# Kernel optimization log

Hardware: AMD Instinct MI355X
Metric: run time of the kernel (lower is better)

The kernel has to match this reference:

```python
import jax, jax.numpy as jnp
import numpy as np

EPS = 1e-15  # matches torch_geometric dense pooling EPS


def gcn_conv(x, src, dst, w, W, b, n):
    # GCNConv(normalize=False): linear first, then weighted scatter-add src->dst, then bias
    h = x @ W
    msg = w[:, None] * h[src]  # [E, out]
    return jax.ops.segment_sum(msg, dst, num_segments=n) + b


def setup_inputs() -> dict:
    key = jax.random.key(0)
    ks = jax.random.split(key, 8)
    N, E, d, k = 12288, 393216, 256, 16
    x = jax.random.normal(ks[0], (N, d), dtype=jnp.float32)
    edge_index = jax.random.randint(ks[1], (2, E), 0, N, dtype=jnp.int32)
    edge_weight = jax.random.uniform(ks[2], (E,), dtype=jnp.float32)
    sc = 1.0 / np.sqrt(d).astype(np.float32)
    W1 = jax.random.normal(ks[3], (d, d), dtype=jnp.float32) * sc
    b1 = jnp.zeros((d,), jnp.float32)
    W2 = jax.random.normal(ks[4], (d, d), dtype=jnp.float32) * sc
    b2 = jnp.zeros((d,), jnp.float32)
    Wm = jax.random.normal(ks[5], (d, k), dtype=jnp.float32) * sc
    bm = jnp.zeros((k,), jnp.float32)
    return dict(x=x, edge_weight=edge_weight, W1=W1, b1=b1, W2=W2, b2=b2,
                Wm=Wm, bm=bm, edge_index=edge_index)


def reference(x, edge_weight, W1, b1, W2, b2, Wm, bm, edge_index):
    src, dst = edge_index[0], edge_index[1]
    n = x.shape[0]
    # message-passing stack: GCNConv -> ReLU -> GCNConv -> ReLU
    h = jax.nn.relu(gcn_conv(x, src, dst, edge_weight, W1, b1, n))
    h = jax.nn.relu(gcn_conv(h, src, dst, edge_weight, W2, b2, n))
    # cluster MLP (single Linear, Identity activations)
    s_logits = h @ Wm + bm  # [N, k]
    # to_dense_adj(edge_index, edge_attr=edge_weight): dense [N, N]
    adj = jnp.zeros((n, n), x.dtype).at[src, dst].add(edge_weight)
    # just_balance_pool (batch of 1)
    s = jax.nn.softmax(s_logits, axis=-1)  # [N, k]
    out = s.T @ h              # pooled features (unused by module output)
    out_adj = s.T @ adj @ s    # pooled adjacency (unused by module output)
    gram = s.T @ s             # [k, k]
    k = s.shape[-1]
    b_loss = -jnp.trace(jnp.sqrt(gram + EPS)) / jnp.sqrt(jnp.float32(n * k))
    return s, b_loss
```

## Files before the change

### kernel.cpp

```cpp
#include <hip/hip_runtime.h>
#include <hip/hip_bf16.h>
#include <hip/hip_fp16.h>

#define D 256
#define KCL 16
#define EPS 1e-15f
#define PAD 128

typedef __attribute__((ext_vector_type(8))) short short8;
typedef __attribute__((ext_vector_type(4))) float f32x4;

__device__ __forceinline__ short bfhi(float v) {
    __hip_bfloat16 b = __float2bfloat16(v);
    return __builtin_bit_cast(short, b);
}
__device__ __forceinline__ float bf2f(short s) {
    __hip_bfloat16 b = __builtin_bit_cast(__hip_bfloat16, s);
    return __bfloat162float(b);
}

__global__ __launch_bounds__(256) void setup_k(const float* __restrict__ W1,
                                               const float* __restrict__ W2,
                                               short* __restrict__ Wt1h, short* __restrict__ Wt1l,
                                               short* __restrict__ Wt2h, short* __restrict__ Wt2l,
                                               const int* __restrict__ src,
                                               const int* __restrict__ dst,
                                               const float* __restrict__ ew,
                                               int* __restrict__ deg,
                                               int2* __restrict__ edges, int E) {
    int b = blockIdx.x;
    if (b < 512) {
        const float* W = (b < 256) ? W1 : W2;
        short* Th = (b < 256) ? Wt1h : Wt2h;
        short* Tl = (b < 256) ? Wt1l : Wt2l;
        int c = b & 255;
        int k = threadIdx.x;
        float v = W[(size_t)k * D + c];
        short h = bfhi(v);
        Th[(size_t)c * D + k] = h;
        Tl[(size_t)c * D + k] = bfhi(v - bf2f(h));
    } else {
        int e = (b - 512) * 256 + threadIdx.x;
        if (e < E) {
            int d = dst[e];
            int slot = atomicAdd(&deg[d], 1);
            if (slot < PAD)
                edges[(size_t)d * PAD + slot] = make_int2(src[e], __float_as_int(ew[e]));
        }
    }
}

#define GBM 64
#define APAD 40
__global__ __launch_bounds__(256) void gemm_k(const float* __restrict__ A,
                                              const short* __restrict__ Bth,
                                              const short* __restrict__ Btl,
                                              __half* __restrict__ C) {
    __shared__ short Ah[GBM][APAD];
    __shared__ short Al[GBM][APAD];
    int tid = threadIdx.x;
    int lane = tid & 63, w = tid >> 6;
    int bm = blockIdx.x * GBM, bn = blockIdx.y * 64;
    f32x4 acc[4];
#pragma unroll
    for (int i = 0; i < 4; ++i) acc[i] = (f32x4){0.f, 0.f, 0.f, 0.f};

    int r  = tid >> 2;
    int cc = (tid & 3) * 8;
    int ar = w * 16 + (lane & 15);
    int kq = (lane >> 4) * 8;

    for (int kk = 0; kk < D; kk += 32) {
        const float* ap = &A[(size_t)(bm + r) * D + kk + cc];
        float4 v0 = *(const float4*)ap;
        float4 v1 = *(const float4*)(ap + 4);
        float vv[8] = {v0.x, v0.y, v0.z, v0.w, v1.x, v1.y, v1.z, v1.w};
        short8 hi, lo;
#pragma unroll
        for (int j = 0; j < 8; ++j) {
            short h = bfhi(vv[j]);
            hi[j] = h;
            lo[j] = bfhi(vv[j] - bf2f(h));
        }
        __syncthreads();
        *(short8*)&Ah[r][cc] = hi;
        *(short8*)&Al[r][cc] = lo;
        __syncthreads();

        short8 a_h = *(const short8*)&Ah[ar][kq];
        short8 a_l = *(const short8*)&Al[ar][kq];
#pragma unroll
        for (int nf = 0; nf < 4; ++nf) {
            int col = bn + nf * 16 + (lane & 15);
            short8 b_h = *(const short8*)&Bth[(size_t)col * D + kk + kq];
            short8 b_l = *(const short8*)&Btl[(size_t)col * D + kk + kq];
            acc[nf] = __builtin_amdgcn_mfma_f32_16x16x32_bf16(a_h, b_h, acc[nf], 0, 0, 0);
            acc[nf] = __builtin_amdgcn_mfma_f32_16x16x32_bf16(a_h, b_l, acc[nf], 0, 0, 0);
            acc[nf] = __builtin_amdgcn_mfma_f32_16x16x32_bf16(a_l, b_h, acc[nf], 0, 0, 0);
        }
    }
    int rbase = bm + w * 16 + (lane >> 4) * 4;
    int cb = bn + (lane & 15);
#pragma unroll
    for (int nf = 0; nf < 4; ++nf)
#pragma unroll
        for (int rr = 0; rr < 4; ++rr)
            C[(size_t)(rbase + rr) * D + cb + nf * 16] = __float2half(acc[nf][rr]);
}

__global__ __launch_bounds__(128) void spmm_k(const __half* __restrict__ h,
                                              const int2* __restrict__ edges,
                                              const int* __restrict__ deg,
                                              const float* __restrict__ bias,
                                              float* __restrict__ out) {
    int node = blockIdx.x;
    int t = threadIdx.x;
    int n = min(deg[node], PAD);
    __shared__ int2 se[PAD];
    if (t < n) se[t] = edges[(size_t)node * PAD + t];
    __syncthreads();
    const __half2* h2 = (const __half2*)h;
    float acc0 = 0.f, acc1 = 0.f;
    int i = 0;
    for (; i + 4 <= n; i += 4) {
        int2 e0 = se[i], e1 = se[i + 1], e2 = se[i + 2], e3 = se[i + 3];
        float2 a0 = __half22float2(h2[(size_t)e0.x * (D / 2) + t]);
        float2 a1 = __half22float2(h2[(size_t)e1.x * (D / 2) + t]);
        float2 a2 = __half22float2(h2[(size_t)e2.x * (D / 2) + t]);
        float2 a3 = __half22float2(h2[(size_t)e3.x * (D / 2) + t]);
        float w0 = __int_as_float(e0.y), w1 = __int_as_float(e1.y);
        float w2 = __int_as_float(e2.y), w3 = __int_as_float(e3.y);
        acc0 = fmaf(w0, a0.x, acc0); acc1 = fmaf(w0, a0.y, acc1);
        acc0 = fmaf(w1, a1.x, acc0); acc1 = fmaf(w1, a1.y, acc1);
        acc0 = fmaf(w2, a2.x, acc0); acc1 = fmaf(w2, a2.y, acc1);
        acc0 = fmaf(w3, a3.x, acc0); acc1 = fmaf(w3, a3.y, acc1);
    }
    for (; i < n; ++i) {
        int2 e = se[i];
        float2 a = __half22float2(h2[(size_t)e.x * (D / 2) + t]);
        float wv = __int_as_float(e.y);
        acc0 = fmaf(wv, a.x, acc0); acc1 = fmaf(wv, a.y, acc1);
    }
    float2 bv = *(const float2*)&bias[2 * t];
    *(float2*)&out[(size_t)node * D + 2 * t] =
        make_float2(fmaxf(acc0 + bv.x, 0.f), fmaxf(acc1 + bv.y, 0.f));
}

__global__ __launch_bounds__(256) void cluster_k(const float* __restrict__ h,
                                                 const float* __restrict__ Wm,
                                                 const float* __restrict__ bmv,
                                                 float* __restrict__ s_out,
                                                 float* __restrict__ partial) {
    __shared__ float dssq[4][KCL];
    int tid = threadIdx.x;
    int wave = tid >> 6, lane = tid & 63;
    int node = blockIdx.x * 4 + wave;

    float4 hv = *(const float4*)&h[(size_t)node * D + lane * 4];
    float p[KCL];
#pragma unroll
    for (int j = 0; j < KCL; ++j) p[j] = 0.f;
    const float* hp = (const float*)&hv;
#pragma unroll
    for (int u = 0; u < 4; ++u) {
        float hval = hp[u];
        const float4* wrow = (const float4*)&Wm[(size_t)(lane * 4 + u) * KCL];
#pragma unroll
        for (int q = 0; q < 4; ++q) {
            float4 wv = wrow[q];
            p[q * 4 + 0] = fmaf(hval, wv.x, p[q * 4 + 0]);
            p[q * 4 + 1] = fmaf(hval, wv.y, p[q * 4 + 1]);
            p[q * 4 + 2] = fmaf(hval, wv.z, p[q * 4 + 2]);
            p[q * 4 + 3] = fmaf(hval, wv.w, p[q * 4 + 3]);
        }
    }
#pragma unroll
    for (int off = 32; off; off >>= 1)
#pragma unroll
        for (int j = 0; j < KCL; ++j) p[j] += __shfl_xor(p[j], off, 64);
    if (lane == 0) {
        float mx = -1e30f;
#pragma unroll
        for (int j = 0; j < KCL; ++j) { p[j] += bmv[j]; mx = fmaxf(mx, p[j]); }
        float sum = 0.f;
#pragma unroll
        for (int j = 0; j < KCL; ++j) { p[j] = __expf(p[j] - mx); sum += p[j]; }
        float inv = 1.f / sum;
        float* so = &s_out[(size_t)node * KCL];
#pragma unroll
        for (int q = 0; q < 4; ++q) {
            float s0 = p[q*4+0] * inv, s1 = p[q*4+1] * inv;
            float s2 = p[q*4+2] * inv, s3 = p[q*4+3] * inv;
            *(float4*)&so[q * 4] = make_float4(s0, s1, s2, s3);
            dssq[wave][q*4+0] = s0 * s0; dssq[wave][q*4+1] = s1 * s1;
            dssq[wave][q*4+2] = s2 * s2; dssq[wave][q*4+3] = s3 * s3;
        }
    }
    __syncthreads();
    if (tid < KCL)
        partial[(size_t)blockIdx.x * KCL + tid] =
            dssq[0][tid] + dssq[1][tid] + dssq[2][tid] + dssq[3][tid];
}

__global__ __launch_bounds__(1024) void final_k(const float* __restrict__ partial,
                                                float* __restrict__ loss_out,
                                                int nblk, int N) {
    int tid = threadIdx.x;
    int total = nblk * KCL;
    float acc = 0.f;
    for (int idx = tid; idx < total; idx += 1024)
        acc += partial[idx];
    int j = tid & 15, g = tid >> 4;
    __shared__ float red[64][KCL + 1];
    red[g][j] = acc;
    __syncthreads();
    if (tid < KCL) {
        float v = 0.f;
#pragma unroll
        for (int gg = 0; gg < 64; ++gg) v += red[gg][tid];
        red[0][tid] = sqrtf(v + EPS);
    }
    __syncthreads();
    if (tid == 0) {
        float sum = 0.f;
#pragma unroll
        for (int jj = 0; jj < KCL; ++jj) sum += red[0][jj];
        loss_out[0] = -sum / sqrtf((float)N * (float)KCL);
    }
}

extern "C" void kernel_launch(void* const* d_in, const int* in_sizes, int n_in,
                              void* d_out, int out_size, void* d_ws, size_t ws_size,
                              hipStream_t stream) {
    const float* x  = (const float*)d_in[0];
    const float* ew = (const float*)d_in[1];
    const float* W1 = (const float*)d_in[2];
    const float* b1 = (const float*)d_in[3];
    const float* W2 = (const float*)d_in[4];
    const float* b2 = (const float*)d_in[5];
    const float* Wm = (const float*)d_in[6];
    const float* bm = (const float*)d_in[7];
    const int*   ei = (const int*)d_in[8];

    const int N = in_sizes[0] / D;
    const int E = in_sizes[1];
    const int* src = ei;
    const int* dst = ei + E;

    float* out = (float*)d_out;

    char* ws = (char*)d_ws;
    __half* G    = (__half*)ws;       ws += (size_t)N * D * 2;
    float* H     = (float*)ws;        ws += (size_t)N * D * 4;
    int*   deg   = (int*)ws;          ws += (size_t)N * 4;
    int2*  edges = (int2*)ws;         ws += (size_t)N * PAD * 8;
    short* Wt1h  = (short*)ws;        ws += (size_t)D * D * 2;
    short* Wt1l  = (short*)ws;        ws += (size_t)D * D * 2;
    short* Wt2h  = (short*)ws;        ws += (size_t)D * D * 2;
    short* Wt2l  = (short*)ws;        ws += (size_t)D * D * 2;
    float* partial = (float*)ws;      ws += (size_t)(N / 4) * KCL * 4;

    hipMemsetAsync(deg, 0, (size_t)N * 4, stream);
    int gE = (E + 255) / 256;
    setup_k<<<512 + gE, 256, 0, stream>>>(W1, W2, Wt1h, Wt1l, Wt2h, Wt2l,
                                          src, dst, ew, deg, edges, E);

    dim3 ggrid(N / GBM, 4);
    gemm_k<<<ggrid, 256, 0, stream>>>(x, Wt1h, Wt1l, G);
    spmm_k<<<N, 128, 0, stream>>>(G, edges, deg, b1, H);
    gemm_k<<<ggrid, 256, 0, stream>>>(H, Wt2h, Wt2l, G);
    spmm_k<<<N, 128, 0, stream>>>(G, edges, deg, b2, H);
    cluster_k<<<N / 4, 256, 0, stream>>>(H, Wm, bm, out, partial);
    final_k<<<1, 1024, 0, stream>>>(partial, out + (size_t)N * KCL, N / 4, N);
}
```

Baseline: 240.4 us.

## Switch GEMMs to single fp16 MFMA, store hidden in fp16, fuse cluster into SpMM

The GEMMs now use a single fp16 MFMA per tile in place of the three-term bf16 split, and the weights are stored as fp16. The first SpMM writes fp16 activations that the second GEMM loads directly. The second SpMM is fused with the cluster linear plus softmax, which removes one kernel and the fp32 H round trip. final_k now computes the squared sums straight from s, so the partial buffer is gone. The cost is lower precision in both GEMMs and in the intermediate activations.

```diff
diff --git a/kernel.cpp b/kernel.cpp
--- a/kernel.cpp
+++ b/kernel.cpp
@@ -8,21 +8,13 @@
 #define PAD 128
 
 typedef __attribute__((ext_vector_type(8))) short short8;
+typedef __attribute__((ext_vector_type(8))) _Float16 half8;
 typedef __attribute__((ext_vector_type(4))) float f32x4;
-
-__device__ __forceinline__ short bfhi(float v) {
-    __hip_bfloat16 b = __float2bfloat16(v);
-    return __builtin_bit_cast(short, b);
-}
-__device__ __forceinline__ float bf2f(short s) {
-    __hip_bfloat16 b = __builtin_bit_cast(__hip_bfloat16, s);
-    return __bfloat162float(b);
-}
 
 __global__ __launch_bounds__(256) void setup_k(const float* __restrict__ W1,
                                                const float* __restrict__ W2,
-                                               short* __restrict__ Wt1h, short* __restrict__ Wt1l,
-                                               short* __restrict__ Wt2h, short* __restrict__ Wt2l,
+                                               __half* __restrict__ Wt1,
+                                               __half* __restrict__ Wt2,
                                                const int* __restrict__ src,
                                                const int* __restrict__ dst,
                                                const float* __restrict__ ew,
@@ -31,14 +23,10 @@
     int b = blockIdx.x;
     if (b < 512) {
         const float* W = (b < 256) ? W1 : W2;
-        short* Th = (b < 256) ? Wt1h : Wt2h;
-        short* Tl = (b < 256) ? Wt1l : Wt2l;
+        __half* T = (b < 256) ? Wt1 : Wt2;
         int c = b & 255;
         int k = threadIdx.x;
-        float v = W[(size_t)k * D + c];
-        short h = bfhi(v);
-        Th[(size_t)c * D + k] = h;
-        Tl[(size_t)c * D + k] = bfhi(v - bf2f(h));
+        T[(size_t)c * D + k] = __float2half(W[(size_t)k * D + c]);
     } else {
         int e = (b - 512) * 256 + threadIdx.x;
         if (e < E) {
@@ -50,17 +38,30 @@
     }
 }
 
-#define GBM 64
-#define APAD 40
-__global__ __launch_bounds__(256) void gemm_k(const float* __restrict__ A,
-                                              const short* __restrict__ Bth,
-                                              const short* __restrict__ Btl,
+__device__ __forceinline__ short8 ld8h(const float* p) {
+    float4 v0 = *(const float4*)p;
+    float4 v1 = *(const float4*)(p + 4);
+    float vv[8] = {v0.x, v0.y, v0.z, v0.w, v1.x, v1.y, v1.z, v1.w};
+    short8 o;
+#pragma unroll
+    for (int j = 0; j < 8; ++j) {
+        _Float16 h = (_Float16)vv[j];
+        o[j] = __builtin_bit_cast(short, h);
+    }
+    return o;
+}
+__device__ __forceinline__ short8 ld8h(const __half* p) {
+    return *(const short8*)p;
+}
+
+template<typename T>
+__global__ __launch_bounds__(256) void gemm_k(const T* __restrict__ A,
+                                              const __half* __restrict__ Bt,
                                               __half* __restrict__ C) {
-    __shared__ short Ah[GBM][APAD];
-    __shared__ short Al[GBM][APAD];
+    __shared__ short Ah[64][40];
     int tid = threadIdx.x;
     int lane = tid & 63, w = tid >> 6;
-    int bm = blockIdx.x * GBM, bn = blockIdx.y * 64;
+    int bm = blockIdx.x * 64, bn = blockIdx.y * 64;
     f32x4 acc[4];
 #pragma unroll
     for (int i = 0; i < 4; ++i) acc[i] = (f32x4){0.f, 0.f, 0.f, 0.f};
@@ -71,32 +72,18 @@
     int kq = (lane >> 4) * 8;
 
     for (int kk = 0; kk < D; kk += 32) {
-        const float* ap = &A[(size_t)(bm + r) * D + kk + cc];
-        float4 v0 = *(const float4*)ap;
-        float4 v1 = *(const float4*)(ap + 4);
-        float vv[8] = {v0.x, v0.y, v0.z, v0.w, v1.x, v1.y, v1.z, v1.w};
-        short8 hi, lo;
-#pragma unroll
-        for (int j = 0; j < 8; ++j) {
-            short h = bfhi(vv[j]);
-            hi[j] = h;
-            lo[j] = bfhi(vv[j] - bf2f(h));
-        }
+        short8 a8 = ld8h(&A[(size_t)(bm + r) * D + kk + cc]);
         __syncthreads();
-        *(short8*)&Ah[r][cc] = hi;
-        *(short8*)&Al[r][cc] = lo;
+        *(short8*)&Ah[r][cc] = a8;
         __syncthreads();
 
-        short8 a_h = *(const short8*)&Ah[ar][kq];
-        short8 a_l = *(const short8*)&Al[ar][kq];
+        half8 av = __builtin_bit_cast(half8, *(const short8*)&Ah[ar][kq]);
 #pragma unroll
         for (int nf = 0; nf < 4; ++nf) {
             int col = bn + nf * 16 + (lane & 15);
-            short8 b_h = *(const short8*)&Bth[(size_t)col * D + kk + kq];
-            short8 b_l = *(const short8*)&Btl[(size_t)col * D + kk + kq];
-            acc[nf] = __builtin_amdgcn_mfma_f32_16x16x32_bf16(a_h, b_h, acc[nf], 0, 0, 0);
-            acc[nf] = __builtin_amdgcn_mfma_f32_16x16x32_bf16(a_h, b_l, acc[nf], 0, 0, 0);
-            acc[nf] = __builtin_amdgcn_mfma_f32_16x16x32_bf16(a_l, b_h, acc[nf], 0, 0, 0);
+            half8 bv = __builtin_bit_cast(half8,
+                        *(const short8*)&Bt[(size_t)col * D + kk + kq]);
+            acc[nf] = __builtin_amdgcn_mfma_f32_16x16x32_f16(av, bv, acc[nf], 0, 0, 0);
         }
     }
     int rbase = bm + w * 16 + (lane >> 4) * 4;
@@ -112,7 +99,7 @@
                                               const int2* __restrict__ edges,
                                               const int* __restrict__ deg,
                                               const float* __restrict__ bias,
-                                              float* __restrict__ out) {
+                                              __half* __restrict__ out) {
     int node = blockIdx.x;
     int t = threadIdx.x;
     int n = min(deg[node], PAD);
@@ -142,74 +129,99 @@
         acc0 = fmaf(wv, a.x, acc0); acc1 = fmaf(wv, a.y, acc1);
     }
     float2 bv = *(const float2*)&bias[2 * t];
-    *(float2*)&out[(size_t)node * D + 2 * t] =
-        make_float2(fmaxf(acc0 + bv.x, 0.f), fmaxf(acc1 + bv.y, 0.f));
-}
-
-__global__ __launch_bounds__(256) void cluster_k(const float* __restrict__ h,
-                                                 const float* __restrict__ Wm,
-                                                 const float* __restrict__ bmv,
-                                                 float* __restrict__ s_out,
-                                                 float* __restrict__ partial) {
-    __shared__ float dssq[4][KCL];
-    int tid = threadIdx.x;
-    int wave = tid >> 6, lane = tid & 63;
-    int node = blockIdx.x * 4 + wave;
-
-    float4 hv = *(const float4*)&h[(size_t)node * D + lane * 4];
-    float p[KCL];
-#pragma unroll
-    for (int j = 0; j < KCL; ++j) p[j] = 0.f;
-    const float* hp = (const float*)&hv;
-#pragma unroll
-    for (int u = 0; u < 4; ++u) {
-        float hval = hp[u];
-        const float4* wrow = (const float4*)&Wm[(size_t)(lane * 4 + u) * KCL];
-#pragma unroll
-        for (int q = 0; q < 4; ++q) {
-            float4 wv = wrow[q];
-            p[q * 4 + 0] = fmaf(hval, wv.x, p[q * 4 + 0]);
-            p[q * 4 + 1] = fmaf(hval, wv.y, p[q * 4 + 1]);
-            p[q * 4 + 2] = fmaf(hval, wv.z, p[q * 4 + 2]);
-            p[q * 4 + 3] = fmaf(hval, wv.w, p[q * 4 + 3]);
+    float f0 = fmaxf(acc0 + bv.x, 0.f), f1 = fmaxf(acc1 + bv.y, 0.f);
+    ((__half2*)out)[(size_t)node * (D / 2) + t] = __float22half2_rn(make_float2(f0, f1));
+}
+
+__global__ __launch_bounds__(128) void spmm_cluster_k(const __half* __restrict__ h,
+                                                      const int2* __restrict__ edges,
+                                                      const int* __restrict__ deg,
+                                                      const float* __restrict__ bias,
+                                                      const float* __restrict__ Wm,
+                                                      const float* __restrict__ bmv,
+                                                      float* __restrict__ s_out) {
+    int node = blockIdx.x;
+    int t = threadIdx.x;
+    int n = min(deg[node], PAD);
+    __shared__ int2 se[PAD];
+    if (t < n) se[t] = edges[(size_t)node * PAD + t];
+    __syncthreads();
+    const __half2* h2 = (const __half2*)h;
+    float acc0 = 0.f, acc1 = 0.f;
+    int i = 0;
+    for (; i + 4 <= n; i += 4) {
+        int2 e0 = se[i], e1 = se[i + 1], e2 = se[i + 2], e3 = se[i + 3];
+        float2 a0 = __half22float2(h2[(size_t)e0.x * (D / 2) + t]);
+        float2 a1 = __half22float2(h2[(size_t)e1.x * (D / 2) + t]);
+        float2 a2 = __half22float2(h2[(size_t)e2.x * (D / 2) + t]);
+        float2 a3 = __half22float2(h2[(size_t)e3.x * (D / 2) + t]);
+        float w0 = __int_as_float(e0.y), w1 = __int_as_float(e1.y);
+        float w2 = __int_as_float(e2.y), w3 = __int_as_float(e3.y);
+        acc0 = fmaf(w0, a0.x, acc0); acc1 = fmaf(w0, a0.y, acc1);
+        acc0 = fmaf(w1, a1.x, acc0); acc1 = fmaf(w1, a1.y, acc1);
+        acc0 = fmaf(w2, a2.x, acc0); acc1 = fmaf(w2, a2.y, acc1);
+        acc0 = fmaf(w3, a3.x, acc0); acc1 = fmaf(w3, a3.y, acc1);
+    }
+    for (; i < n; ++i) {
+        int2 e = se[i];
+        float2 a = __half22float2(h2[(size_t)e.x * (D / 2) + t]);
+        float wv = __int_as_float(e.y);
+        acc0 = fmaf(wv, a.x, acc0); acc1 = fmaf(wv, a.y, acc1);
+    }
+    float2 bv = *(const float2*)&bias[2 * t];
+    float f0 = fmaxf(acc0 + bv.x, 0.f), f1 = fmaxf(acc1 + bv.y, 0.f);
+
+    float pl[KCL];
+    const float4* w0 = (const float4*)&Wm[(size_t)(2 * t) * KCL];
+    const float4* w1 = (const float4*)&Wm[(size_t)(2 * t + 1) * KCL];
+#pragma unroll
+    for (int q = 0; q < 4; ++q) {
+        float4 a = w0[q], b = w1[q];
+        pl[q * 4 + 0] = f0 * a.x + f1 * b.x;
+        pl[q * 4 + 1] = f0 * a.y + f1 * b.y;
+        pl[q * 4 + 2] = f0 * a.z + f1 * b.z;
+        pl[q * 4 + 3] = f0 * a.w + f1 * b.w;
+    }
+#pragma unroll
+    for (int off = 32; off; off >>= 1)
+#pragma unroll
+        for (int j = 0; j < KCL; ++j) pl[j] += __shfl_xor(pl[j], off, 64);
+    __shared__ float xw[2][KCL];
+    int wv = t >> 6, ln = t & 63;
+    if (ln == 0) {
+#pragma unroll
+        for (int j = 0; j < KCL; ++j) xw[wv][j] = pl[j];
+    }
+    __syncthreads();
+    if (t == 0) {
+        float p[KCL];
+        float mx = -1e30f;
+#pragma unroll
+        for (int j = 0; j < KCL; ++j) {
+            p[j] = xw[0][j] + xw[1][j] + bmv[j];
+            mx = fmaxf(mx, p[j]);
         }
-    }
-#pragma unroll
-    for (int off = 32; off; off >>= 1)
-#pragma unroll
-        for (int j = 0; j < KCL; ++j) p[j] += __shfl_xor(p[j], off, 64);
-    if (lane == 0) {
-        float mx = -1e30f;
-#pragma unroll
-        for (int j = 0; j < KCL; ++j) { p[j] += bmv[j]; mx = fmaxf(mx, p[j]); }
         float sum = 0.f;
 #pragma unroll
         for (int j = 0; j < KCL; ++j) { p[j] = __expf(p[j] - mx); sum += p[j]; }
         float inv = 1.f / sum;
         float* so = &s_out[(size_t)node * KCL];
 #pragma unroll
-        for (int q = 0; q < 4; ++q) {
-            float s0 = p[q*4+0] * inv, s1 = p[q*4+1] * inv;
-            float s2 = p[q*4+2] * inv, s3 = p[q*4+3] * inv;
-            *(float4*)&so[q * 4] = make_float4(s0, s1, s2, s3);
-            dssq[wave][q*4+0] = s0 * s0; dssq[wave][q*4+1] = s1 * s1;
-            dssq[wave][q*4+2] = s2 * s2; dssq[wave][q*4+3] = s3 * s3;
-        }
-    }
-    __syncthreads();
-    if (tid < KCL)
-        partial[(size_t)blockIdx.x * KCL + tid] =
-            dssq[0][tid] + dssq[1][tid] + dssq[2][tid] + dssq[3][tid];
-}
-
-__global__ __launch_bounds__(1024) void final_k(const float* __restrict__ partial,
-                                                float* __restrict__ loss_out,
-                                                int nblk, int N) {
+        for (int q = 0; q < 4; ++q)
+            *(float4*)&so[q * 4] = make_float4(p[q*4+0] * inv, p[q*4+1] * inv,
+                                               p[q*4+2] * inv, p[q*4+3] * inv);
+    }
+}
+
+__global__ __launch_bounds__(1024) void final_k(const float* __restrict__ s,
+                                                float* __restrict__ loss_out, int N) {
     int tid = threadIdx.x;
-    int total = nblk * KCL;
+    int total = N * KCL;
     float acc = 0.f;
-    for (int idx = tid; idx < total; idx += 1024)
-        acc += partial[idx];
+    for (int idx = tid; idx < total; idx += 1024) {
+        float v = s[idx];
+        acc = fmaf(v, v, acc);
+    }
     int j = tid & 15, g = tid >> 4;
     __shared__ float red[64][KCL + 1];
     red[g][j] = acc;
@@ -251,25 +263,21 @@
 
     char* ws = (char*)d_ws;
     __half* G    = (__half*)ws;       ws += (size_t)N * D * 2;
-    float* H     = (float*)ws;        ws += (size_t)N * D * 4;
+    __half* H1   = (__half*)ws;       ws += (size_t)N * D * 2;
     int*   deg   = (int*)ws;          ws += (size_t)N * 4;
     int2*  edges = (int2*)ws;         ws += (size_t)N * PAD * 8;
-    short* Wt1h  = (short*)ws;        ws += (size_t)D * D * 2;
-    short* Wt1l  = (short*)ws;        ws += (size_t)D * D * 2;
-    short* Wt2h  = (short*)ws;        ws += (size_t)D * D * 2;
-    short* Wt2l  = (short*)ws;        ws += (size_t)D * D * 2;
-    float* partial = (float*)ws;      ws += (size_t)(N / 4) * KCL * 4;
+    __half* Wt1  = (__half*)ws;       ws += (size_t)D * D * 2;
+    __half* Wt2  = (__half*)ws;       ws += (size_t)D * D * 2;
 
     hipMemsetAsync(deg, 0, (size_t)N * 4, stream);
     int gE = (E + 255) / 256;
-    setup_k<<<512 + gE, 256, 0, stream>>>(W1, W2, Wt1h, Wt1l, Wt2h, Wt2l,
+    setup_k<<<512 + gE, 256, 0, stream>>>(W1, W2, Wt1, Wt2,
                                           src, dst, ew, deg, edges, E);
 
-    dim3 ggrid(N / GBM, 4);
-    gemm_k<<<ggrid, 256, 0, stream>>>(x, Wt1h, Wt1l, G);
-    spmm_k<<<N, 128, 0, stream>>>(G, edges, deg, b1, H);
-    gemm_k<<<ggrid, 256, 0, stream>>>(H, Wt2h, Wt2l, G);
-    spmm_k<<<N, 128, 0, stream>>>(G, edges, deg, b2, H);
-    cluster_k<<<N / 4, 256, 0, stream>>>(H, Wm, bm, out, partial);
-    final_k<<<1, 1024, 0, stream>>>(partial, out + (size_t)N * KCL, N / 4, N);
-}
+    dim3 ggrid(N / 64, 4);
+    gemm_k<float><<<ggrid, 256, 0, stream>>>(x, Wt1, G);
+    spmm_k<<<N, 128, 0, stream>>>(G, edges, deg, b1, H1);
+    gemm_k<__half><<<ggrid, 256, 0, stream>>>(H1, Wt2, G);
+    spmm_cluster_k<<<N, 128, 0, stream>>>(G, edges, deg, b2, Wm, bm, out);
+    final_k<<<1, 1024, 0, stream>>>(out, out + (size_t)N * KCL, N);
+}
```

New measurement: 250.5 us. 4.2% more time.
